# Optimization experiments

Hardware: AMD Instinct MI355X
Metric: run time of the kernel (lower is better)

The kernel has to match this reference:

```python
import jax, jax.numpy as jnp
import numpy as np

EMBED_DIM = 1024
NUM_HEADS = 16
HEAD_DIM = EMBED_DIM // NUM_HEADS
BATCH = 2
SEQ = 2048


def setup_inputs() -> dict:
    key = jax.random.key(0)
    ks = jax.random.split(key, 9)
    s = 1.0 / np.sqrt(EMBED_DIM)
    return {
        "x": jax.random.normal(ks[0], (BATCH, SEQ, EMBED_DIM), jnp.float32),
        "mask": jnp.ones((BATCH, SEQ), jnp.int32),
        "Wq": jax.random.normal(ks[1], (EMBED_DIM, EMBED_DIM), jnp.float32) * s,
        "bq": jax.random.normal(ks[2], (EMBED_DIM,), jnp.float32) * s,
        "Wk": jax.random.normal(ks[3], (EMBED_DIM, EMBED_DIM), jnp.float32) * s,
        "bk": jax.random.normal(ks[4], (EMBED_DIM,), jnp.float32) * s,
        "Wv": jax.random.normal(ks[5], (EMBED_DIM, EMBED_DIM), jnp.float32) * s,
        "bv": jax.random.normal(ks[6], (EMBED_DIM,), jnp.float32) * s,
        "Wo": jax.random.normal(ks[7], (EMBED_DIM, EMBED_DIM), jnp.float32) * s,
        "bo": jax.random.normal(ks[8], (EMBED_DIM,), jnp.float32) * s,
    }


def reference(x, mask, Wq, bq, Wk, bk, Wv, bv, Wo, bo):
    B, S, E = x.shape
    H, D = NUM_HEADS, HEAD_DIM
    # torch Linear: y = x @ W.T + b
    q = (x @ Wq.T + bq).reshape(B, S, H, D).transpose(0, 2, 1, 3)  # [B,H,S,D]
    k = (x @ Wk.T + bk).reshape(B, S, H, D).transpose(0, 2, 1, 3)
    v = (x @ Wv.T + bv).reshape(B, S, H, D).transpose(0, 2, 1, 3)
    scores = jnp.einsum("bhqd,bhkd->bhqk", q, k) / jnp.sqrt(jnp.float32(D))
    # mask: [B,S] -> [B,1,1,S]; fill masked positions with -1e9
    scores = jnp.where(mask[:, None, None, :] == 0, jnp.float32(-1e9), scores)
    probs = jax.nn.softmax(scores, axis=-1)
    # dropout omitted: original stores a float and would crash; eval semantics = identity
    attn = jnp.einsum("bhqk,bhkd->bhqd", probs, v)  # [B,H,S,D]
    attn = attn.transpose(0, 2, 1, 3).reshape(B, S, E)
    return attn @ Wo.T + bo
```

## Files before the change

kernel.cpp:

```cpp
#include <hip/hip_runtime.h>
#include <stdint.h>

#define S_LEN 2048
#define EMB   1024
#define NH    16
#define HD    64
#define BM 128
#define BN 128
#define BK 64

typedef __bf16 bf16x8 __attribute__((ext_vector_type(8)));
typedef short  short4v __attribute__((ext_vector_type(4)));
typedef unsigned int uint2v __attribute__((ext_vector_type(2)));
typedef float  floatx4 __attribute__((ext_vector_type(4)));

#if defined(__has_builtin)
#if __has_builtin(__builtin_amdgcn_mfma_f32_16x16x16bf16_1k)
#define HAVE_MFMA16 1
#endif
#if __has_builtin(__builtin_amdgcn_exp2f)
#define EXP2F(x) __builtin_amdgcn_exp2f(x)
#endif
#endif
#ifndef EXP2F
#define EXP2F(x) exp2f(x)
#endif

#define QSCALE 0.1803368801111204f

__device__ __forceinline__ unsigned short f2bf(float f) {
  unsigned u = __builtin_bit_cast(unsigned, f);
  u += 0x7fffu + ((u >> 16) & 1u);
  return (unsigned short)(u >> 16);
}

__global__ __launch_bounds__(256) void cvt_all(const float* __restrict__ x,
                                               const float* __restrict__ Wq,
                                               const float* __restrict__ Wk,
                                               const float* __restrict__ Wv,
                                               const float* __restrict__ Wo,
                                               unsigned short* __restrict__ xb,
                                               unsigned short* __restrict__ Wqb,
                                               unsigned short* __restrict__ Wkb,
                                               unsigned short* __restrict__ Wvb,
                                               unsigned short* __restrict__ Wob) {
  int blk = blockIdx.x;
  const float* s; unsigned short* d; int off;
  if (blk < 4096)      { s = x;  d = xb;  off = blk; }
  else if (blk < 5120) { s = Wq; d = Wqb; off = blk - 4096; }
  else if (blk < 6144) { s = Wk; d = Wkb; off = blk - 5120; }
  else if (blk < 7168) { s = Wv; d = Wvb; off = blk - 6144; }
  else                 { s = Wo; d = Wob; off = blk - 7168; }
  int i = (off * 256 + threadIdx.x) * 4;
  float4 v = *(const float4*)(s + i);
  ushort4 o;
  o.x = f2bf(v.x); o.y = f2bf(v.y); o.z = f2bf(v.z); o.w = f2bf(v.w);
  *(ushort4*)(d + i) = o;
}

__device__ __forceinline__ void stage16(const void* g, void* l) {
  __builtin_amdgcn_global_load_lds(
      (const __attribute__((address_space(1))) void*)g,
      (__attribute__((address_space(3))) void*)l, 16, 0, 0);
}

__device__ __forceinline__ void gemm128(const unsigned short* __restrict__ A,
                                        const unsigned short* __restrict__ Bm,
                                        const float* __restrict__ bias, float scale,
                                        void* __restrict__ outp, int mode,
                                        unsigned short* As, unsigned short* Bs) {
  const int tid  = threadIdx.x;
  const int lane = tid & 63;
  const int wave = tid >> 6;
  const int m16  = lane & 15;
  const int quad = lane >> 4;
  const int m0 = blockIdx.x * BM;
  const int n0 = blockIdx.y * BN;
  const int wrow = (wave >> 1) * 64;
  const int wcol = (wave & 1) * 64;
  const int K = 1024, N = 1024;

  floatx4 acc[4][4];
  for (int i = 0; i < 4; ++i)
    for (int j = 0; j < 4; ++j) acc[i][j] = floatx4{0.f, 0.f, 0.f, 0.f};

  for (int k0 = 0; k0 < K; k0 += BK) {
    __syncthreads();
    for (int i = 0; i < 4; ++i) {
      int c   = i * 256 + tid;
      int row = c >> 3;
      int col = (c & 7) << 3;
      stage16(A  + (size_t)(m0 + row) * K + k0 + col,
              (char*)As + (size_t)(i * 256 + wave * 64) * 16);
      stage16(Bm + (size_t)(n0 + row) * K + k0 + col,
              (char*)Bs + (size_t)(i * 256 + wave * 64) * 16);
    }
    __syncthreads();
    for (int kk = 0; kk < 2; ++kk) {
      bf16x8 af[4], bfr[4];
      for (int ti = 0; ti < 4; ++ti)
        af[ti] = *(const bf16x8*)(As + (wrow + ti * 16 + m16) * BK + kk * 32 + quad * 8);
      for (int tj = 0; tj < 4; ++tj)
        bfr[tj] = *(const bf16x8*)(Bs + (wcol + tj * 16 + m16) * BK + kk * 32 + quad * 8);
      if (mode == 2) {
        for (int ti = 0; ti < 4; ++ti)
          for (int tj = 0; tj < 4; ++tj)
            acc[ti][tj] = __builtin_amdgcn_mfma_f32_16x16x32_bf16(bfr[tj], af[ti], acc[ti][tj], 0, 0, 0);
      } else {
        for (int ti = 0; ti < 4; ++ti)
          for (int tj = 0; tj < 4; ++tj)
            acc[ti][tj] = __builtin_amdgcn_mfma_f32_16x16x32_bf16(af[ti], bfr[tj], acc[ti][tj], 0, 0, 0);
      }
    }
  }

  if (mode == 2) {
    for (int tj = 0; tj < 4; ++tj) {
      for (int reg = 0; reg < 4; ++reg) {
        int n = n0 + wcol + tj * 16 + quad * 4 + reg;
        int hh = n >> 6, d = n & 63;
        float bv = bias[n];
        for (int ti = 0; ti < 4; ++ti) {
          int m = m0 + wrow + ti * 16 + m16;
          int b = m >> 11, s = m & 2047;
          ((unsigned short*)outp)[((size_t)(b * NH + hh) * HD + d) * S_LEN + s] =
              f2bf(acc[ti][tj][reg] + bv);
        }
      }
    }
    return;
  }

  for (int tj = 0; tj < 4; ++tj) {
    int n = n0 + wcol + tj * 16 + m16;
    float bv = bias[n];
    for (int ti = 0; ti < 4; ++ti) {
      for (int reg = 0; reg < 4; ++reg) {
        int m = m0 + wrow + ti * 16 + quad * 4 + reg;
        float v = (acc[ti][tj][reg] + bv) * scale;
        if (mode == 0) {
          ((float*)outp)[(size_t)m * N + n] = v;
        } else {
          int b = m >> 11, s = m & 2047, hh = n >> 6, d = n & 63;
          ((unsigned short*)outp)[((size_t)(b * NH + hh) * S_LEN + s) * HD + d] = f2bf(v);
        }
      }
    }
  }
}

__global__ __launch_bounds__(256) void qkv_gemm(const unsigned short* __restrict__ xb,
                                                const unsigned short* __restrict__ Wqb,
                                                const unsigned short* __restrict__ Wkb,
                                                const unsigned short* __restrict__ Wvb,
                                                const float* __restrict__ bq,
                                                const float* __restrict__ bk,
                                                const float* __restrict__ bv,
                                                unsigned short* __restrict__ Qb,
                                                unsigned short* __restrict__ Kb,
                                                unsigned short* __restrict__ Vtb) {
  __shared__ unsigned short As[BM * BK];
  __shared__ unsigned short Bs[BN * BK];
  int z = blockIdx.z;
  const unsigned short* Bm = (z == 0) ? Wqb : (z == 1) ? Wkb : Wvb;
  const float* bias        = (z == 0) ? bq  : (z == 1) ? bk  : bv;
  unsigned short* outp     = (z == 0) ? Qb  : (z == 1) ? Kb  : Vtb;
  float scale = (z == 0) ? QSCALE : 1.0f;
  gemm128(xb, Bm, bias, scale, outp, (z == 2) ? 2 : 1, As, Bs);
}

__global__ __launch_bounds__(256) void out_gemm(const unsigned short* __restrict__ Ab,
                                                const unsigned short* __restrict__ Wob,
                                                const float* __restrict__ bo,
                                                float* __restrict__ out) {
  __shared__ unsigned short As[64 * BK];
  __shared__ unsigned short Bs[128 * BK];
  const int tid  = threadIdx.x;
  const int lane = tid & 63;
  const int wave = tid >> 6;
  const int m16  = lane & 15;
  const int quad = lane >> 4;
  const int m0 = blockIdx.x * 64;
  const int n0 = blockIdx.y * 128;
  const int wrow = (wave >> 1) * 32;
  const int wcol = (wave & 1) * 64;
  const int K = 1024, N = 1024;

  floatx4 acc[2][4];
  for (int i = 0; i < 2; ++i)
    for (int j = 0; j < 4; ++j) acc[i][j] = floatx4{0.f, 0.f, 0.f, 0.f};

  for (int k0 = 0; k0 < K; k0 += BK) {
    __syncthreads();
    for (int i = 0; i < 2; ++i) {
      int c = i * 256 + tid;
      int row = c >> 3, col = (c & 7) << 3;
      stage16(Ab + (size_t)(m0 + row) * K + k0 + col,
              (char*)As + (size_t)(i * 256 + wave * 64) * 16);
    }
    for (int i = 0; i < 4; ++i) {
      int c = i * 256 + tid;
      int row = c >> 3, col = (c & 7) << 3;
      stage16(Wob + (size_t)(n0 + row) * K + k0 + col,
              (char*)Bs + (size_t)(i * 256 + wave * 64) * 16);
    }
    __syncthreads();
    for (int kk = 0; kk < 2; ++kk) {
      bf16x8 af[2], bfr[4];
      for (int ti = 0; ti < 2; ++ti)
        af[ti] = *(const bf16x8*)(As + (wrow + ti * 16 + m16) * BK + kk * 32 + quad * 8);
      for (int tj = 0; tj < 4; ++tj)
        bfr[tj] = *(const bf16x8*)(Bs + (wcol + tj * 16 + m16) * BK + kk * 32 + quad * 8);
      for (int ti = 0; ti < 2; ++ti)
        for (int tj = 0; tj < 4; ++tj)
          acc[ti][tj] = __builtin_amdgcn_mfma_f32_16x16x32_bf16(af[ti], bfr[tj], acc[ti][tj], 0, 0, 0);
    }
  }

  for (int tj = 0; tj < 4; ++tj) {
    int n = n0 + wcol + tj * 16 + m16;
    float bv = bo[n];
    for (int ti = 0; ti < 2; ++ti)
      for (int reg = 0; reg < 4; ++reg) {
        int m = m0 + wrow + ti * 16 + quad * 4 + reg;
        out[(size_t)m * N + n] = acc[ti][tj][reg] + bv;
      }
  }
}

__global__ __launch_bounds__(512, 2) void attn_kernel(const unsigned short* __restrict__ Qb,
                                                      const unsigned short* __restrict__ Kb,
                                                      const unsigned short* __restrict__ Vtb,
                                                      const int* __restrict__ mask,
                                                      unsigned short* __restrict__ attnb) {
  __shared__ unsigned short Ks[128 * 64];
  __shared__ unsigned short Vts[64 * 128];
  __shared__ float mb[128];
#ifndef HAVE_MFMA16
  __shared__ unsigned short Pq[8 * 16 * 72];
#endif

  const int tid  = threadIdx.x;
  const int lane = tid & 63;
  const int wave = tid >> 6;
  const int m16  = lane & 15;
  const int quad = lane >> 4;
  const int bh = blockIdx.x;
  const int qt = blockIdx.y;
  const int b  = bh >> 4;
  const int h  = bh & 15;
  const int q0 = qt * 128;
  const size_t head = (size_t)bh * S_LEN * HD;

  bf16x8 qf[2];
  {
    const unsigned short* qrow = Qb + head + (size_t)(q0 + wave * 16 + m16) * HD;
    qf[0] = *(const bf16x8*)(qrow + quad * 8);
    qf[1] = *(const bf16x8*)(qrow + 32 + quad * 8);
  }

  const int krow = tid >> 3, kch = tid & 7;
  const unsigned short* kg = Kb + head + (size_t)krow * HD + kch * 8;
  unsigned short* kl = Ks + krow * 64 + (kch ^ (krow & 7)) * 8;
  const int vrow = tid >> 4, vch = tid & 15;
  const unsigned short* vg = Vtb + head + (size_t)vrow * S_LEN + vch * 8;
  unsigned short* vl = Vts + vrow * 128 + (vch ^ (vrow & 7)) * 8;

  float m_run = -1e30f, l_run = 0.f;
  floatx4 acc_o[4];
  for (int ti = 0; ti < 4; ++ti) acc_o[ti] = floatx4{0.f, 0.f, 0.f, 0.f};

  uint4 kp0 = *(const uint4*)(kg);
  uint4 kp1 = *(const uint4*)(kg + 64 * HD);
  uint4 vp0 = *(const uint4*)(vg);
  uint4 vp1 = *(const uint4*)(vg + 32 * S_LEN);
  int   mp  = (tid < 128) ? mask[b * S_LEN + tid] : 1;

  const int xs = m16 & 7;

  for (int kb = 0; kb < 16; ++kb) {
    __syncthreads();
    *(uint4*)kl = kp0;  *(uint4*)(kl + 64 * 64) = kp1;
    *(uint4*)vl = vp0;  *(uint4*)(vl + 32 * 128) = vp1;
    if (tid < 128) mb[tid] = (mp == 0) ? -1e9f : 0.f;
    __syncthreads();

    {
      int kvn = (kb + 1 < 16) ? (kb + 1) * 128 : 0;
      kp0 = *(const uint4*)(kg + (size_t)kvn * HD);
      kp1 = *(const uint4*)(kg + (size_t)(kvn + 64) * HD);
      vp0 = *(const uint4*)(vg + kvn);
      vp1 = *(const uint4*)(vg + 32 * S_LEN + kvn);
      if (tid < 128) mp = mask[b * S_LEN + kvn + tid];
    }

    for (int hf = 0; hf < 2; ++hf) {
      floatx4 acc_s[4];
      for (int tj = 0; tj < 4; ++tj) acc_s[tj] = floatx4{0.f, 0.f, 0.f, 0.f};
      for (int kk = 0; kk < 2; ++kk)
        for (int tj = 0; tj < 4; ++tj) {
          bf16x8 kf = *(const bf16x8*)&Ks[(hf * 64 + tj * 16 + m16) * 64 +
                                          (((kk * 4 + quad) ^ xs) << 3)];
          acc_s[tj] = __builtin_amdgcn_mfma_f32_16x16x32_bf16(kf, qf[kk], acc_s[tj], 0, 0, 0);
        }

      float s[16];
      for (int t = 0; t < 4; ++t) {
        float4 mv = *(const float4*)&mb[hf * 64 + t * 16 + quad * 4];
        s[t * 4 + 0] = acc_s[t][0] + mv.x;
        s[t * 4 + 1] = acc_s[t][1] + mv.y;
        s[t * 4 + 2] = acc_s[t][2] + mv.z;
        s[t * 4 + 3] = acc_s[t][3] + mv.w;
      }
      float mloc = fmaxf(fmaxf(fmaxf(s[0], s[1]), fmaxf(s[2], s[3])),
                         fmaxf(fmaxf(s[4], s[5]), fmaxf(s[6], s[7])));
      float mloc2 = fmaxf(fmaxf(fmaxf(s[8], s[9]), fmaxf(s[10], s[11])),
                          fmaxf(fmaxf(s[12], s[13]), fmaxf(s[14], s[15])));
      mloc = fmaxf(mloc, mloc2);
      mloc = fmaxf(mloc, __shfl_xor(mloc, 16));
      mloc = fmaxf(mloc, __shfl_xor(mloc, 32));

      if (__any(mloc > m_run)) {
        float mnew = fmaxf(m_run, mloc);
        float alpha = EXP2F(m_run - mnew);
        m_run = mnew;
        l_run *= alpha;
        for (int ti = 0; ti < 4; ++ti)
          for (int reg = 0; reg < 4; ++reg) acc_o[ti][reg] *= alpha;
      }

      unsigned up[8];
      float sl = 0.f;
      for (int i = 0; i < 8; ++i) {
        float p0 = EXP2F(s[2 * i] - m_run);
        float p1 = EXP2F(s[2 * i + 1] - m_run);
        unsigned u0 = __builtin_bit_cast(unsigned, p0) + 0x8000u;
        unsigned u1 = __builtin_bit_cast(unsigned, p1) + 0x8000u;
        up[i] = __builtin_amdgcn_perm(u1, u0, 0x07060302);
        sl += __builtin_bit_cast(float, u0 & 0xffff0000u) +
              __builtin_bit_cast(float, u1 & 0xffff0000u);
      }
      sl += __shfl_xor(sl, 16);
      sl += __shfl_xor(sl, 32);
      l_run += sl;

#ifdef HAVE_MFMA16
      for (int ti = 0; ti < 4; ++ti)
        for (int c = 0; c < 4; ++c) {
          short4v vf = *(const short4v*)&Vts[(ti * 16 + m16) * 128 +
                                             (((hf * 8 + 2 * c + (quad >> 1)) ^ xs) << 3) +
                                             ((quad & 1) << 2)];
          short4v Pb = __builtin_bit_cast(short4v, uint2v{up[2 * c], up[2 * c + 1]});
          acc_o[ti] = __builtin_amdgcn_mfma_f32_16x16x16bf16_1k(vf, Pb, acc_o[ti], 0, 0, 0);
        }
#else
      unsigned short* Pw = Pq + wave * 16 * 72;
      for (int t = 0; t < 4; ++t) {
        *(unsigned*)&Pw[m16 * 72 + t * 16 + quad * 4]     = up[2 * t];
        *(unsigned*)&Pw[m16 * 72 + t * 16 + quad * 4 + 2] = up[2 * t + 1];
      }
      for (int kk = 0; kk < 2; ++kk) {
        bf16x8 pf = *(const bf16x8*)&Pw[m16 * 72 + kk * 32 + quad * 8];
        for (int ti = 0; ti < 4; ++ti) {
          bf16x8 vf = *(const bf16x8*)&Vts[(ti * 16 + m16) * 128 +
                                           (((hf * 8 + kk * 4 + quad) ^ xs) << 3)];
          acc_o[ti] = __builtin_amdgcn_mfma_f32_16x16x32_bf16(vf, pf, acc_o[ti], 0, 0, 0);
        }
      }
#endif
    }
  }

  float rl = 1.f / l_run;
  int orow = q0 + wave * 16 + m16;
  for (int ti = 0; ti < 4; ++ti) {
    ushort4 o;
    o.x = f2bf(acc_o[ti][0] * rl);
    o.y = f2bf(acc_o[ti][1] * rl);
    o.z = f2bf(acc_o[ti][2] * rl);
    o.w = f2bf(acc_o[ti][3] * rl);
    int e = h * HD + ti * 16 + quad * 4;
    *(ushort4*)&attnb[((size_t)(b * S_LEN + orow)) * EMB + e] = o;
  }
}

extern "C" void kernel_launch(void* const* d_in, const int* in_sizes, int n_in,
                              void* d_out, int out_size, void* d_ws, size_t ws_size,
                              hipStream_t stream) {
  const float* x  = (const float*)d_in[0];
  const int* mask = (const int*)d_in[1];
  const float* Wq = (const float*)d_in[2];
  const float* bq = (const float*)d_in[3];
  const float* Wk = (const float*)d_in[4];
  const float* bk = (const float*)d_in[5];
  const float* Wv = (const float*)d_in[6];
  const float* bv = (const float*)d_in[7];
  const float* Wo = (const float*)d_in[8];
  const float* bo = (const float*)d_in[9];
  float* out = (float*)d_out;

  char* ws = (char*)d_ws;
  unsigned short* xb  = (unsigned short*)(ws);
  unsigned short* Wqb = (unsigned short*)(ws + 8388608);
  unsigned short* Wkb = (unsigned short*)(ws + 10485760);
  unsigned short* Wvb = (unsigned short*)(ws + 12582912);
  unsigned short* Wob = (unsigned short*)(ws + 14680064);
  unsigned short* Qb  = (unsigned short*)(ws + 16777216);
  unsigned short* Kbb = (unsigned short*)(ws + 25165824);
  unsigned short* Vtb = (unsigned short*)(ws + 33554432);
  unsigned short* Ab  = (unsigned short*)(ws + 41943040);

  cvt_all<<<dim3(8192), dim3(256), 0, stream>>>(x, Wq, Wk, Wv, Wo, xb, Wqb, Wkb, Wvb, Wob);
  qkv_gemm<<<dim3(32, 8, 3), dim3(256), 0, stream>>>(xb, Wqb, Wkb, Wvb, bq, bk, bv, Qb, Kbb, Vtb);
  attn_kernel<<<dim3(32, 16), dim3(512), 0, stream>>>(Qb, Kbb, Vtb, mask, Ab);
  out_gemm<<<dim3(64, 8), dim3(256), 0, stream>>>(Ab, Wob, bo, out);
}
```

Measured before the change: 228.8 us.

## Merge attention softmax halves, skip mask bias when unmasked, vectorize Q/K stores

The attention loop now computes both 64-key score halves before a single max/rescale step, so each 128-key block needs one online-softmax update instead of two. A ballot-derived flag lets the mask-bias add be skipped when no key in the block is masked. The Q/K projection epilogue swaps operand order so each lane writes four packed bf16 values at once instead of scattered 16-bit stores. Round-to-nearest-even bf16 conversion is replaced with a cheaper round-half-up, which changes rounding slightly. Holding 32 score registers at once raises register pressure.

```diff
diff --git a/kernel.cpp b/kernel.cpp
--- a/kernel.cpp
+++ b/kernel.cpp
@@ -32,6 +32,14 @@
   unsigned u = __builtin_bit_cast(unsigned, f);
   u += 0x7fffu + ((u >> 16) & 1u);
   return (unsigned short)(u >> 16);
+}
+__device__ __forceinline__ unsigned short f2bf_hu(float f) {
+  return (unsigned short)((__builtin_bit_cast(unsigned, f) + 0x8000u) >> 16);
+}
+__device__ __forceinline__ unsigned packbf2(float a, float b) {
+  unsigned ua = __builtin_bit_cast(unsigned, a) + 0x8000u;
+  unsigned ub = __builtin_bit_cast(unsigned, b) + 0x8000u;
+  return __builtin_amdgcn_perm(ub, ua, 0x07060302);
 }
 
 __global__ __launch_bounds__(256) void cvt_all(const float* __restrict__ x,
@@ -102,7 +110,7 @@
         af[ti] = *(const bf16x8*)(As + (wrow + ti * 16 + m16) * BK + kk * 32 + quad * 8);
       for (int tj = 0; tj < 4; ++tj)
         bfr[tj] = *(const bf16x8*)(Bs + (wcol + tj * 16 + m16) * BK + kk * 32 + quad * 8);
-      if (mode == 2) {
+      if (mode != 0) {
         for (int ti = 0; ti < 4; ++ti)
           for (int tj = 0; tj < 4; ++tj)
             acc[ti][tj] = __builtin_amdgcn_mfma_f32_16x16x32_bf16(bfr[tj], af[ti], acc[ti][tj], 0, 0, 0);
@@ -112,6 +120,26 @@
             acc[ti][tj] = __builtin_amdgcn_mfma_f32_16x16x32_bf16(af[ti], bfr[tj], acc[ti][tj], 0, 0, 0);
       }
     }
+  }
+
+  if (mode == 1) {
+    for (int ti = 0; ti < 4; ++ti) {
+      int m = m0 + wrow + ti * 16 + m16;
+      int b = m >> 11, ss = m & 2047;
+      for (int tj = 0; tj < 4; ++tj) {
+        int n = n0 + wcol + tj * 16 + quad * 4;
+        int hh = n >> 6, d = n & 63;
+        float4 b4 = *(const float4*)(bias + n);
+        float v0 = (acc[ti][tj][0] + b4.x) * scale;
+        float v1 = (acc[ti][tj][1] + b4.y) * scale;
+        float v2 = (acc[ti][tj][2] + b4.z) * scale;
+        float v3 = (acc[ti][tj][3] + b4.w) * scale;
+        uint2v pk{packbf2(v0, v1), packbf2(v2, v3)};
+        *(uint2v*)((unsigned short*)outp +
+                   ((size_t)(b * NH + hh) * S_LEN + ss) * HD + d) = pk;
+      }
+    }
+    return;
   }
 
   if (mode == 2) {
@@ -122,9 +150,9 @@
         float bv = bias[n];
         for (int ti = 0; ti < 4; ++ti) {
           int m = m0 + wrow + ti * 16 + m16;
-          int b = m >> 11, s = m & 2047;
-          ((unsigned short*)outp)[((size_t)(b * NH + hh) * HD + d) * S_LEN + s] =
-              f2bf(acc[ti][tj][reg] + bv);
+          int b = m >> 11, ss = m & 2047;
+          ((unsigned short*)outp)[((size_t)(b * NH + hh) * HD + d) * S_LEN + ss] =
+              f2bf_hu(acc[ti][tj][reg] + bv);
         }
       }
     }
@@ -134,18 +162,11 @@
   for (int tj = 0; tj < 4; ++tj) {
     int n = n0 + wcol + tj * 16 + m16;
     float bv = bias[n];
-    for (int ti = 0; ti < 4; ++ti) {
+    for (int ti = 0; ti < 4; ++ti)
       for (int reg = 0; reg < 4; ++reg) {
         int m = m0 + wrow + ti * 16 + quad * 4 + reg;
-        float v = (acc[ti][tj][reg] + bv) * scale;
-        if (mode == 0) {
-          ((float*)outp)[(size_t)m * N + n] = v;
-        } else {
-          int b = m >> 11, s = m & 2047, hh = n >> 6, d = n & 63;
-          ((unsigned short*)outp)[((size_t)(b * NH + hh) * S_LEN + s) * HD + d] = f2bf(v);
-        }
-      }
-    }
+        ((float*)outp)[(size_t)m * N + n] = acc[ti][tj][reg] + bv;
+      }
   }
 }
 
@@ -236,6 +257,7 @@
   __shared__ unsigned short Ks[128 * 64];
   __shared__ unsigned short Vts[64 * 128];
   __shared__ float mb[128];
+  __shared__ int zf[2];
 #ifndef HAVE_MFMA16
   __shared__ unsigned short Pq[8 * 16 * 72];
 #endif
@@ -283,6 +305,10 @@
     *(uint4*)kl = kp0;  *(uint4*)(kl + 64 * 64) = kp1;
     *(uint4*)vl = vp0;  *(uint4*)(vl + 32 * 128) = vp1;
     if (tid < 128) mb[tid] = (mp == 0) ? -1e9f : 0.f;
+    if (wave < 2) {
+      unsigned long long z = __ballot(mp == 0);
+      if (lane == 0) zf[wave] = (z != 0ull) ? 1 : 0;
+    }
     __syncthreads();
 
     {
@@ -293,57 +319,66 @@
       vp1 = *(const uint4*)(vg + 32 * S_LEN + kvn);
       if (tid < 128) mp = mask[b * S_LEN + kvn + tid];
     }
-
-    for (int hf = 0; hf < 2; ++hf) {
-      floatx4 acc_s[4];
-      for (int tj = 0; tj < 4; ++tj) acc_s[tj] = floatx4{0.f, 0.f, 0.f, 0.f};
+    const bool dobias = (zf[0] | zf[1]) != 0;
+
+    floatx4 acc_s[2][4];
+    for (int hf = 0; hf < 2; ++hf)
+      for (int tj = 0; tj < 4; ++tj) acc_s[hf][tj] = floatx4{0.f, 0.f, 0.f, 0.f};
+    for (int hf = 0; hf < 2; ++hf)
       for (int kk = 0; kk < 2; ++kk)
         for (int tj = 0; tj < 4; ++tj) {
           bf16x8 kf = *(const bf16x8*)&Ks[(hf * 64 + tj * 16 + m16) * 64 +
                                           (((kk * 4 + quad) ^ xs) << 3)];
-          acc_s[tj] = __builtin_amdgcn_mfma_f32_16x16x32_bf16(kf, qf[kk], acc_s[tj], 0, 0, 0);
+          acc_s[hf][tj] = __builtin_amdgcn_mfma_f32_16x16x32_bf16(kf, qf[kk], acc_s[hf][tj], 0, 0, 0);
         }
 
-      float s[16];
-      for (int t = 0; t < 4; ++t) {
-        float4 mv = *(const float4*)&mb[hf * 64 + t * 16 + quad * 4];
-        s[t * 4 + 0] = acc_s[t][0] + mv.x;
-        s[t * 4 + 1] = acc_s[t][1] + mv.y;
-        s[t * 4 + 2] = acc_s[t][2] + mv.z;
-        s[t * 4 + 3] = acc_s[t][3] + mv.w;
-      }
-      float mloc = fmaxf(fmaxf(fmaxf(s[0], s[1]), fmaxf(s[2], s[3])),
-                         fmaxf(fmaxf(s[4], s[5]), fmaxf(s[6], s[7])));
-      float mloc2 = fmaxf(fmaxf(fmaxf(s[8], s[9]), fmaxf(s[10], s[11])),
-                          fmaxf(fmaxf(s[12], s[13]), fmaxf(s[14], s[15])));
-      mloc = fmaxf(mloc, mloc2);
-      mloc = fmaxf(mloc, __shfl_xor(mloc, 16));
-      mloc = fmaxf(mloc, __shfl_xor(mloc, 32));
-
-      if (__any(mloc > m_run)) {
-        float mnew = fmaxf(m_run, mloc);
-        float alpha = EXP2F(m_run - mnew);
-        m_run = mnew;
-        l_run *= alpha;
-        for (int ti = 0; ti < 4; ++ti)
-          for (int reg = 0; reg < 4; ++reg) acc_o[ti][reg] *= alpha;
-      }
-
+    float sx[32];
+    if (dobias) {
+      for (int hf = 0; hf < 2; ++hf)
+        for (int t = 0; t < 4; ++t) {
+          float4 mv = *(const float4*)&mb[hf * 64 + t * 16 + quad * 4];
+          sx[hf * 16 + t * 4 + 0] = acc_s[hf][t][0] + mv.x;
+          sx[hf * 16 + t * 4 + 1] = acc_s[hf][t][1] + mv.y;
+          sx[hf * 16 + t * 4 + 2] = acc_s[hf][t][2] + mv.z;
+          sx[hf * 16 + t * 4 + 3] = acc_s[hf][t][3] + mv.w;
+        }
+    } else {
+      for (int hf = 0; hf < 2; ++hf)
+        for (int t = 0; t < 4; ++t)
+          for (int r = 0; r < 4; ++r)
+            sx[hf * 16 + t * 4 + r] = acc_s[hf][t][r];
+    }
+
+    float t16[16];
+    for (int i = 0; i < 16; ++i) t16[i] = fmaxf(sx[i], sx[16 + i]);
+    float t8[8];
+    for (int i = 0; i < 8; ++i) t8[i] = fmaxf(t16[i], t16[8 + i]);
+    float mloc = fmaxf(fmaxf(fmaxf(t8[0], t8[1]), fmaxf(t8[2], t8[3])),
+                       fmaxf(fmaxf(t8[4], t8[5]), fmaxf(t8[6], t8[7])));
+    mloc = fmaxf(mloc, __shfl_xor(mloc, 16));
+    mloc = fmaxf(mloc, __shfl_xor(mloc, 32));
+
+    if (__any(mloc > m_run)) {
+      float mnew = fmaxf(m_run, mloc);
+      float alpha = EXP2F(m_run - mnew);
+      m_run = mnew;
+      l_run *= alpha;
+      for (int ti = 0; ti < 4; ++ti)
+        for (int reg = 0; reg < 4; ++reg) acc_o[ti][reg] *= alpha;
+    }
+
+    float sl = 0.f;
+    for (int hf = 0; hf < 2; ++hf) {
       unsigned up[8];
-      float sl = 0.f;
       for (int i = 0; i < 8; ++i) {
-        float p0 = EXP2F(s[2 * i] - m_run);
-        float p1 = EXP2F(s[2 * i + 1] - m_run);
+        float p0 = EXP2F(sx[hf * 16 + 2 * i] - m_run);
+        float p1 = EXP2F(sx[hf * 16 + 2 * i + 1] - m_run);
         unsigned u0 = __builtin_bit_cast(unsigned, p0) + 0x8000u;
         unsigned u1 = __builtin_bit_cast(unsigned, p1) + 0x8000u;
         up[i] = __builtin_amdgcn_perm(u1, u0, 0x07060302);
         sl += __builtin_bit_cast(float, u0 & 0xffff0000u) +
               __builtin_bit_cast(float, u1 & 0xffff0000u);
       }
-      sl += __shfl_xor(sl, 16);
-      sl += __shfl_xor(sl, 32);
-      l_run += sl;
-
 #ifdef HAVE_MFMA16
       for (int ti = 0; ti < 4; ++ti)
         for (int c = 0; c < 4; ++c) {
@@ -369,16 +404,19 @@
       }
 #endif
     }
+    sl += __shfl_xor(sl, 16);
+    sl += __shfl_xor(sl, 32);
+    l_run += sl;
   }
 
   float rl = 1.f / l_run;
   int orow = q0 + wave * 16 + m16;
   for (int ti = 0; ti < 4; ++ti) {
     ushort4 o;
-    o.x = f2bf(acc_o[ti][0] * rl);
-    o.y = f2bf(acc_o[ti][1] * rl);
-    o.z = f2bf(acc_o[ti][2] * rl);
-    o.w = f2bf(acc_o[ti][3] * rl);
+    o.x = f2bf_hu(acc_o[ti][0] * rl);
+    o.y = f2bf_hu(acc_o[ti][1] * rl);
+    o.z = f2bf_hu(acc_o[ti][2] * rl);
+    o.w = f2bf_hu(acc_o[ti][3] * rl);
     int e = h * HD + ti * 16 + quad * 4;
     *(ushort4*)&attnb[((size_t)(b * S_LEN + orow)) * EMB + e] = o;
   }
```

Result: no change. 233.3 us (+1.9%).
